# Kernel optimization log

Hardware: AMD Instinct MI355X
Metric: run time of the kernel (lower is better)

## Reference

```python
import jax, jax.numpy as jnp
import numpy as np

D_MODEL = 1024
H = 16
D_K = D_MODEL // H


def setup_inputs() -> dict:
    key = jax.random.key(0)
    ks = jax.random.split(key, 8)
    B, S = 4, 2048
    q = jax.random.normal(ks[0], (B, S, D_MODEL), dtype=jnp.float32)
    k = jax.random.normal(ks[1], (B, S, D_MODEL), dtype=jnp.float32)
    v = jax.random.normal(ks[2], (B, S, D_MODEL), dtype=jnp.float32)
    scale = 1.0 / np.sqrt(D_MODEL)
    W_q = jax.random.normal(ks[3], (H, D_MODEL, D_K), dtype=jnp.float32) * scale
    W_k = jax.random.normal(ks[4], (H, D_MODEL, D_K), dtype=jnp.float32) * scale
    W_v = jax.random.normal(ks[5], (H, D_MODEL, D_K), dtype=jnp.float32) * scale
    W_o = jax.random.normal(ks[6], (D_MODEL, H * D_K), dtype=jnp.float32) * scale
    b_o = jax.random.normal(ks[7], (D_MODEL,), dtype=jnp.float32) * 0.01
    return {"q": q, "k": k, "v": v, "W_q": W_q, "W_k": W_k, "W_v": W_v, "W_o": W_o, "b_o": b_o}


def reference(q, k, v, W_q, W_k, W_v, W_o, b_o):
    # Per-head projections: [B,S,D] x [H,D,dk] -> [H,B,S,dk]
    qh = jnp.einsum('bsd,hdk->hbsk', q, W_q)
    kh = jnp.einsum('bsd,hdk->hbsk', k, W_k)
    vh = jnp.einsum('bsd,hdk->hbsk', v, W_v)
    # Scaled dot-product attention (full score matrix, as in original)
    scores = jnp.einsum('hbsk,hbtk->hbst', qh, kh) / jnp.sqrt(jnp.asarray(D_K, qh.dtype))
    attn = jax.nn.softmax(scores, axis=-1)
    out = jnp.einsum('hbst,hbtk->hbsk', attn, vh)  # [H,B,S,dk]
    # torch.cat(chunks along head dim, dim=2): head-major feature concat -> [B,S,H*dk]
    out = jnp.transpose(out, (1, 2, 0, 3)).reshape(q.shape[0], q.shape[1], H * D_K)
    return out @ W_o.T + b_o
```

## Files before the change

kernel.cpp:

```cpp
#include <hip/hip_runtime.h>

#define S_LEN 2048

typedef __attribute__((ext_vector_type(8))) short v8s;
typedef __attribute__((ext_vector_type(4))) short v4s;
typedef __attribute__((ext_vector_type(4))) float f32x4;
typedef __attribute__((ext_vector_type(4))) unsigned short v4us;
typedef __attribute__((ext_vector_type(4))) unsigned int v4u;

static __device__ __forceinline__ unsigned short f2bf(float x){
  unsigned u = __builtin_bit_cast(unsigned, x);
  u = (u + 0x7fffu + ((u >> 16) & 1u)) >> 16;
  return (unsigned short)u;
}

static __device__ __forceinline__ unsigned pk2(float a, float b){
  unsigned ua = __builtin_bit_cast(unsigned, a) + 0x8000u;
  unsigned ub = __builtin_bit_cast(unsigned, b) + 0x8000u;
  return __builtin_amdgcn_perm(ub, ua, 0x07060302u);
}

static __device__ __forceinline__ void gload16(const void* g, void* l){
  __builtin_amdgcn_global_load_lds((const __attribute__((address_space(1))) void*)g,
                                   (__attribute__((address_space(3))) void*)l, 16, 0, 0);
}

static __device__ __forceinline__ unsigned lds_off(const void* p){
  return (unsigned)(unsigned long long)(__attribute__((address_space(3))) const void*)p;
}

__global__ void conv_w(const float* __restrict__ Wq, const float* __restrict__ Wk,
                       const float* __restrict__ Wv, const float* __restrict__ Wo,
                       unsigned short* __restrict__ outW){
  int i = blockIdx.x*256 + threadIdx.x;
  const int stride = gridDim.x*256;
  for(; i < 4*1048576; i += stride){
    if (i < 3*1048576){
      int which = i >> 20;
      int rem = i & 1048575;
      const float* W = which==0 ? Wq : (which==1 ? Wk : Wv);
      float v = W[rem];
      if (which == 0) v *= 0.18033688011112042f;
      int h = rem >> 16, d = (rem >> 6) & 1023, kk = rem & 63;
      outW[(which<<20) + (((h<<6)+kk)<<10) + d] = f2bf(v);
    } else {
      outW[i] = f2bf(Wo[i - 3*1048576]);
    }
  }
}

__global__ __launch_bounds__(256,2) void gemm_proj(
    const float* __restrict__ Aq, const float* __restrict__ Ak, const float* __restrict__ Avv,
    const unsigned short* __restrict__ Wtb,
    unsigned short* __restrict__ C0, unsigned short* __restrict__ C1, unsigned short* __restrict__ C2){
  __shared__ unsigned short Als[128*64];
  __shared__ unsigned short Bls[128*64];
  const int tid = threadIdx.x;
  const int l = tid & 63, w = tid >> 6;
  const int z = blockIdx.z;
  const float* Af = (z==0) ? Aq : ((z==1) ? Ak : Avv);
  unsigned short* Cb = (z==0) ? C0 : ((z==1) ? C1 : C2);
  int lid = blockIdx.y*8 + blockIdx.x;
  int nid = (lid & 7)*64 + (lid >> 3);
  const int tx = nid & 7, ty = nid >> 3;
  const int m0 = ty*128, n0 = tx*128;
  const int wr = w >> 1, wc = w & 1;

  f32x4 zero = {0.f,0.f,0.f,0.f};
  f32x4 acc[4][4];
  #pragma unroll
  for(int i=0;i<4;i++){
    #pragma unroll
    for(int j=0;j<4;j++) acc[i][j] = zero;
  }

  const int xorm = (l&7)<<4;
  const int g8 = (l>>4)<<3;
  const int rsub = l>>3, csub = l&7;
  const float* Abase = Af + m0*1024;
  const unsigned short* Bbase = Wtb + z*1048576 + n0*1024;

  float4 ar[8];
  #pragma unroll
  for(int i=0;i<4;i++){
    int c = w*4+i, r = c*8+rsub;
    const float4* src = (const float4*)(Abase + r*1024 + csub*8);
    ar[2*i] = src[0]; ar[2*i+1] = src[1];
  }

  for(int kt=0; kt<16; ++kt){
    const int k0 = kt*64;
    __builtin_amdgcn_sched_barrier(0);
    #pragma unroll
    for(int i=0;i<4;i++){
      int c = w*4+i, r = c*8+rsub, col = csub ^ (r&7);
      gload16(Bbase + r*1024 + k0 + col*8, (void*)&Bls[c*512]);
    }
    __builtin_amdgcn_sched_barrier(0);
    #pragma unroll
    for(int i=0;i<4;i++){
      int c = w*4+i, r = c*8+rsub;
      v4u o = { pk2(ar[2*i].x, ar[2*i].y), pk2(ar[2*i].z, ar[2*i].w),
                pk2(ar[2*i+1].x, ar[2*i+1].y), pk2(ar[2*i+1].z, ar[2*i+1].w) };
      *(v4u*)&Als[c*512 + rsub*64 + ((csub ^ (r&7))<<3)] = o;
    }
    __builtin_amdgcn_sched_barrier(0);
    if (kt < 15){
      #pragma unroll
      for(int i=0;i<4;i++){
        int c = w*4+i, r = c*8+rsub;
        const float4* src = (const float4*)(Abase + r*1024 + (k0+64) + csub*8);
        ar[2*i] = src[0]; ar[2*i+1] = src[1];
      }
      __builtin_amdgcn_sched_barrier(0);
      asm volatile("s_waitcnt vmcnt(8) lgkmcnt(0)" ::: "memory");
    } else {
      asm volatile("s_waitcnt vmcnt(0) lgkmcnt(0)" ::: "memory");
    }
    __builtin_amdgcn_s_barrier();
    __builtin_amdgcn_sched_barrier(0);

    const char* Ab = (const char*)Als;
    const char* Bb = (const char*)Bls;
    #pragma unroll
    for(int kk=0; kk<2; ++kk){
      v8s af[4], bfr[4];
      #pragma unroll
      for(int mf=0; mf<4; ++mf){
        int rb = (wr*64 + mf*16 + (l&15))*128;
        v4s lo = *(const v4s*)(Ab + rb + ((kk*64 + g8) ^ xorm));
        v4s hi = *(const v4s*)(Ab + rb + ((kk*64 + 32 + g8) ^ xorm));
        af[mf] = __builtin_shufflevector(lo, hi, 0,1,2,3,4,5,6,7);
      }
      #pragma unroll
      for(int nf=0; nf<4; ++nf){
        int rb = (wc*64 + nf*16 + (l&15))*128;
        v4s lo = *(const v4s*)(Bb + rb + ((kk*64 + g8) ^ xorm));
        v4s hi = *(const v4s*)(Bb + rb + ((kk*64 + 32 + g8) ^ xorm));
        bfr[nf] = __builtin_shufflevector(lo, hi, 0,1,2,3,4,5,6,7);
      }
      #pragma unroll
      for(int mf=0; mf<4; ++mf){
        #pragma unroll
        for(int nf=0; nf<4; ++nf)
          acc[mf][nf] = __builtin_amdgcn_mfma_f32_16x16x32_bf16(af[mf], bfr[nf], acc[mf][nf], 0,0,0);
      }
    }
    __builtin_amdgcn_sched_barrier(0);
    __builtin_amdgcn_s_barrier();
  }

  const int g4 = (l>>4)<<2;
  #pragma unroll
  for(int mf=0; mf<4; ++mf){
    int rowb = m0 + wr*64 + mf*16 + g4;
    #pragma unroll
    for(int nf=0; nf<4; ++nf){
      int col = n0 + wc*64 + nf*16 + (l&15);
      #pragma unroll
      for(int r=0;r<4;++r)
        Cb[(rowb+r)*1024 + col] = f2bf(acc[mf][nf][r]);
    }
  }
}

template<int EPI>
__global__ __launch_bounds__(256,2) void gemm_bt(const unsigned short* __restrict__ A,
                                                 const unsigned short* __restrict__ Bt,
                                                 void* __restrict__ Cout,
                                                 const float* __restrict__ bias){
  __shared__ unsigned short Als[128*64];
  __shared__ unsigned short Bls[128*64];
  const int tid = threadIdx.x;
  const int l = tid & 63, w = tid >> 6;
  int lid = blockIdx.y*8 + blockIdx.x;
  int nid = (lid & 7)*64 + (lid >> 3);
  const int tx = nid & 7, ty = nid >> 3;
  const int m0 = ty*128, n0 = tx*128;
  const int wr = w >> 1, wc = w & 1;

  f32x4 zero = {0.f,0.f,0.f,0.f};
  f32x4 acc[4][4];
  #pragma unroll
  for(int i=0;i<4;i++){
    #pragma unroll
    for(int j=0;j<4;j++) acc[i][j] = zero;
  }

  const int xorm = (l&7)<<4;
  const int g8 = (l>>4)<<3;
  const int rsub = l>>3, csub = l&7;
  const unsigned short* Abase = A + m0*1024;
  const unsigned short* Bbase = Bt + n0*1024;

  for(int kt=0; kt<16; ++kt){
    const int k0 = kt*64;
    #pragma unroll
    for(int i=0;i<4;i++){
      int c = w*4+i, r = c*8+rsub, col = csub ^ (r&7);
      gload16(Abase + r*1024 + k0 + col*8, (void*)&Als[c*512]);
    }
    #pragma unroll
    for(int i=0;i<4;i++){
      int c = w*4+i, r = c*8+rsub, col = csub ^ (r&7);
      gload16(Bbase + r*1024 + k0 + col*8, (void*)&Bls[c*512]);
    }
    __syncthreads();
    const char* Ab = (const char*)Als;
    const char* Bb = (const char*)Bls;
    #pragma unroll
    for(int kk=0; kk<2; ++kk){
      v8s af[4], bfr[4];
      #pragma unroll
      for(int mf=0; mf<4; ++mf){
        int rb = (wr*64 + mf*16 + (l&15))*128;
        v4s lo = *(const v4s*)(Ab + rb + ((kk*64 + g8) ^ xorm));
        v4s hi = *(const v4s*)(Ab + rb + ((kk*64 + 32 + g8) ^ xorm));
        af[mf] = __builtin_shufflevector(lo, hi, 0,1,2,3,4,5,6,7);
      }
      #pragma unroll
      for(int nf=0; nf<4; ++nf){
        int rb = (wc*64 + nf*16 + (l&15))*128;
        v4s lo = *(const v4s*)(Bb + rb + ((kk*64 + g8) ^ xorm));
        v4s hi = *(const v4s*)(Bb + rb + ((kk*64 + 32 + g8) ^ xorm));
        bfr[nf] = __builtin_shufflevector(lo, hi, 0,1,2,3,4,5,6,7);
      }
      #pragma unroll
      for(int mf=0; mf<4; ++mf){
        #pragma unroll
        for(int nf=0; nf<4; ++nf)
          acc[mf][nf] = __builtin_amdgcn_mfma_f32_16x16x32_bf16(af[mf], bfr[nf], acc[mf][nf], 0,0,0);
      }
    }
    __syncthreads();
  }

  const int g4 = (l>>4)<<2;
  if (EPI == 0){
    unsigned short* C = (unsigned short*)Cout;
    #pragma unroll
    for(int mf=0; mf<4; ++mf){
      int rowb = m0 + wr*64 + mf*16 + g4;
      #pragma unroll
      for(int nf=0; nf<4; ++nf){
        int col = n0 + wc*64 + nf*16 + (l&15);
        #pragma unroll
        for(int r=0;r<4;++r)
          C[(rowb+r)*1024 + col] = f2bf(acc[mf][nf][r]);
      }
    }
  } else {
    float* C = (float*)Cout;
    #pragma unroll
    for(int mf=0; mf<4; ++mf){
      int rowb = m0 + wr*64 + mf*16 + g4;
      #pragma unroll
      for(int nf=0; nf<4; ++nf){
        int col = n0 + wc*64 + nf*16 + (l&15);
        float bv = bias[col];
        #pragma unroll
        for(int r=0;r<4;++r)
          C[(rowb+r)*1024 + col] = acc[mf][nf][r] + bv;
      }
    }
  }
}

__global__ __launch_bounds__(256,2) void attn_fwd(const unsigned short* __restrict__ Q,
                                                  const unsigned short* __restrict__ K,
                                                  const unsigned short* __restrict__ V,
                                                  unsigned short* __restrict__ O){
  __shared__ unsigned short KVls[2][2][64*64];
  const int tid = threadIdx.x;
  const int l = tid & 63, w = tid >> 6;
  int lid = blockIdx.y*16 + blockIdx.x;
  int nid = (lid & 7)*128 + (lid >> 3);
  const int qb = nid & 15, bh = nid >> 4;
  const int b = bh >> 4, h = bh & 15;
  const int base = b*S_LEN*1024 + h*64;
  const int q0 = qb*128;
  const int xorm = (l&7)<<4, g8 = (l>>4)<<3, g4 = (l>>4)<<2;
  const int rsub = l>>3, csub = l&7;

  auto stage_kv = [&](int kt2, int buf){
    const int k0 = kt2*64;
    #pragma unroll
    for(int i=0;i<2;i++){
      int c = w*2+i, r = c*8+rsub, col = csub ^ (r&7);
      gload16(K + base + (k0+r)*1024 + col*8, (void*)&KVls[buf][0][c*512]);
    }
    #pragma unroll
    for(int i=0;i<2;i++){
      int c = w*2+i;
      int e0 = c*512 + l*8;
      int kg = e0>>10, dg = (e0>>8)&3, kin = (e0>>4)&15, din = e0&15;
      gload16(V + base + (k0 + kg*16 + kin)*1024 + dg*16 + din, (void*)&KVls[buf][1][c*512]);
    }
  };

  #pragma unroll
  for(int i=0;i<4;i++){
    int c = w*4+i, r = c*8+rsub, col = csub ^ (r&7);
    gload16(Q + base + (q0+r)*1024 + col*8, (void*)&KVls[1][0][c*512]);
  }
  stage_kv(0, 0);
  __syncthreads();

  v8s qf[2][2];
  {
    const char* Qb = (const char*)&KVls[1][0][0];
    #pragma unroll
    for(int qh=0; qh<2; ++qh){
      int rb = (w*32 + qh*16 + (l&15))*128;
      #pragma unroll
      for(int t=0;t<2;t++){
        v4s lo = *(const v4s*)(Qb + rb + ((t*64 + g8) ^ xorm));
        v4s hi = *(const v4s*)(Qb + rb + ((t*64 + 32 + g8) ^ xorm));
        qf[qh][t] = __builtin_shufflevector(lo, hi, 0,1,2,3,4,5,6,7);
      }
    }
  }
  __builtin_amdgcn_sched_barrier(0);
  __syncthreads();

  f32x4 zero = {0.f,0.f,0.f,0.f};
  f32x4 oacc[2][4];
  #pragma unroll
  for(int qh=0;qh<2;qh++){
    #pragma unroll
    for(int nf=0;nf<4;nf++) oacc[qh][nf] = zero;
  }
  float lsum[2] = {0.f, 0.f};
  const unsigned vbase0 = lds_off(&KVls[0][1][0]) + l*8;
  const unsigned vbase1 = lds_off(&KVls[1][1][0]) + l*8;

  int cur = 0;
  for(int kt=0; kt<32; ++kt){
    if (kt < 31) stage_kv(kt+1, cur^1);

    const char* Kb = (const char*)&KVls[cur][0][0];
    f32x4 sf[2][4];
    #pragma unroll
    for(int mf=0;mf<4;mf++){
      int rb = (mf*16 + (l&15))*128;
      v8s kf[2];
      #pragma unroll
      for(int t=0;t<2;t++){
        v4s lo = *(const v4s*)(Kb + rb + ((t*64 + g8) ^ xorm));
        v4s hi = *(const v4s*)(Kb + rb + ((t*64 + 32 + g8) ^ xorm));
        kf[t] = __builtin_shufflevector(lo, hi, 0,1,2,3,4,5,6,7);
      }
      #pragma unroll
      for(int qh=0;qh<2;qh++){
        sf[qh][mf] = __builtin_amdgcn_mfma_f32_16x16x32_bf16(kf[0], qf[qh][0], zero, 0,0,0);
        sf[qh][mf] = __builtin_amdgcn_mfma_f32_16x16x32_bf16(kf[1], qf[qh][1], sf[qh][mf], 0,0,0);
      }
    }

    const unsigned vb_sel = cur ? vbase1 : vbase0;
    v4s vtr[2][2][4];
    #define TRR(T,H,N,OFF) asm volatile("ds_read_b64_tr_b16 %0, %1 offset:" #OFF \
                     : "=v"(vtr[T][H][N]) : "v"(vb_sel) : "memory")
    TRR(0,0,0,0);    TRR(0,0,1,512);  TRR(0,0,2,1024); TRR(0,0,3,1536);
    TRR(0,1,0,2048); TRR(0,1,1,2560); TRR(0,1,2,3072); TRR(0,1,3,3584);
    TRR(1,0,0,4096); TRR(1,0,1,4608); TRR(1,0,2,5120); TRR(1,0,3,5632);
    TRR(1,1,0,6144); TRR(1,1,1,6656); TRR(1,1,2,7168); TRR(1,1,3,7680);
    #undef TRR

    v8s pa[2][2];
    #pragma unroll
    for(int qh=0;qh<2;qh++){
      unsigned pd[2][4];
      float ls = 0.f;
      #pragma unroll
      for(int mf=0;mf<4;mf++){
        float e0 = __builtin_amdgcn_exp2f(sf[qh][mf][0]);
        float e1 = __builtin_amdgcn_exp2f(sf[qh][mf][1]);
        float e2 = __builtin_amdgcn_exp2f(sf[qh][mf][2]);
        float e3 = __builtin_amdgcn_exp2f(sf[qh][mf][3]);
        ls += (e0+e1)+(e2+e3);
        int t = mf>>1, hf = mf&1;
        pd[t][hf*2+0] = pk2(e0, e1);
        pd[t][hf*2+1] = pk2(e2, e3);
      }
      lsum[qh] += ls;
      #pragma unroll
      for(int t=0;t<2;t++){
        v4u u = { pd[t][0], pd[t][1], pd[t][2], pd[t][3] };
        pa[qh][t] = __builtin_bit_cast(v8s, u);
      }
    }

    asm volatile("s_waitcnt lgkmcnt(0)" ::: "memory");
    __builtin_amdgcn_sched_barrier(0);
    __builtin_amdgcn_s_setprio(1);
    #pragma unroll
    for(int t=0;t<2;t++){
      #pragma unroll
      for(int nf=0;nf<4;nf++){
        v8s vb = __builtin_shufflevector(vtr[t][0][nf], vtr[t][1][nf], 0,1,2,3,4,5,6,7);
        #pragma unroll
        for(int qh=0;qh<2;qh++)
          oacc[qh][nf] = __builtin_amdgcn_mfma_f32_16x16x32_bf16(pa[qh][t], vb, oacc[qh][nf], 0,0,0);
      }
    }
    __builtin_amdgcn_s_setprio(0);
    __syncthreads();
    cur ^= 1;
  }

  #pragma unroll
  for(int qh=0;qh<2;qh++){
    float s = lsum[qh];
    s += __shfl_xor(s, 16, 64);
    s += __shfl_xor(s, 32, 64);
    float i0 = 1.f/__shfl(s, g4+0, 64);
    float i1 = 1.f/__shfl(s, g4+1, 64);
    float i2 = 1.f/__shfl(s, g4+2, 64);
    float i3 = 1.f/__shfl(s, g4+3, 64);
    const int row = q0 + w*32 + qh*16 + g4;
    #pragma unroll
    for(int nf=0;nf<4;nf++){
      int col = nf*16 + (l&15);
      O[base + (row+0)*1024 + col] = f2bf(oacc[qh][nf][0]*i0);
      O[base + (row+1)*1024 + col] = f2bf(oacc[qh][nf][1]*i1);
      O[base + (row+2)*1024 + col] = f2bf(oacc[qh][nf][2]*i2);
      O[base + (row+3)*1024 + col] = f2bf(oacc[qh][nf][3]*i3);
    }
  }
}

extern "C" void kernel_launch(void* const* d_in, const int* in_sizes, int n_in,
                              void* d_out, int out_size, void* d_ws, size_t ws_size,
                              hipStream_t stream) {
  (void)in_sizes; (void)n_in; (void)out_size;
  const float* q  = (const float*)d_in[0];
  const float* k  = (const float*)d_in[1];
  const float* v  = (const float*)d_in[2];
  const float* Wq = (const float*)d_in[3];
  const float* Wk = (const float*)d_in[4];
  const float* Wv = (const float*)d_in[5];
  const float* Wo = (const float*)d_in[6];
  const float* bo = (const float*)d_in[7];

  if (ws_size < (size_t)37748736*2) return;
  unsigned short* ws  = (unsigned short*)d_ws;
  unsigned short* Qh  = ws;
  unsigned short* Kh  = ws +  8388608;
  unsigned short* Vh  = ws + 16777216;
  unsigned short* AO  = ws + 25165824;
  unsigned short* Wt  = ws + 33554432;
  unsigned short* Wob = Wt + 3145728;

  conv_w<<<dim3(2048), dim3(256), 0, stream>>>(Wq, Wk, Wv, Wo, Wt);

  gemm_proj<<<dim3(8,64,3), dim3(256), 0, stream>>>(q, k, v, Wt, Qh, Kh, Vh);

  attn_fwd<<<dim3(16,64), dim3(256), 0, stream>>>(Qh, Kh, Vh, AO);

  gemm_bt<1><<<dim3(8,64), dim3(256), 0, stream>>>(AO, Wob, d_out, bo);
}
```

Measured before the change: 233.1 us.

## Double-buffer LDS tiles in projection GEMM to overlap loads with MFMA

Result: no change. 231.0 us (-0.9%).

```diff
diff --git a/kernel.cpp b/kernel.cpp
--- a/kernel.cpp
+++ b/kernel.cpp
@@ -53,8 +53,8 @@
     const float* __restrict__ Aq, const float* __restrict__ Ak, const float* __restrict__ Avv,
     const unsigned short* __restrict__ Wtb,
     unsigned short* __restrict__ C0, unsigned short* __restrict__ C1, unsigned short* __restrict__ C2){
-  __shared__ unsigned short Als[128*64];
-  __shared__ unsigned short Bls[128*64];
+  __shared__ unsigned short Als[2][128*64];
+  __shared__ unsigned short Bls[2][128*64];
   const int tid = threadIdx.x;
   const int l = tid & 63, w = tid >> 6;
   const int z = blockIdx.z;
@@ -83,45 +83,61 @@
   float4 ar[8];
   #pragma unroll
   for(int i=0;i<4;i++){
+    int c = w*4+i, r = c*8+rsub, col = csub ^ (r&7);
+    gload16(Bbase + r*1024 + col*8, (void*)&Bls[0][c*512]);
+  }
+  #pragma unroll
+  for(int i=0;i<4;i++){
     int c = w*4+i, r = c*8+rsub;
     const float4* src = (const float4*)(Abase + r*1024 + csub*8);
     ar[2*i] = src[0]; ar[2*i+1] = src[1];
   }
-
+  #pragma unroll
+  for(int i=0;i<4;i++){
+    int c = w*4+i, r = c*8+rsub;
+    v4u o = { pk2(ar[2*i].x, ar[2*i].y), pk2(ar[2*i].z, ar[2*i].w),
+              pk2(ar[2*i+1].x, ar[2*i+1].y), pk2(ar[2*i+1].z, ar[2*i+1].w) };
+    *(v4u*)&Als[0][c*512 + rsub*64 + ((csub ^ (r&7))<<3)] = o;
+  }
+  #pragma unroll
+  for(int i=0;i<4;i++){
+    int c = w*4+i, r = c*8+rsub;
+    const float4* src = (const float4*)(Abase + r*1024 + 64 + csub*8);
+    ar[2*i] = src[0]; ar[2*i+1] = src[1];
+  }
+  asm volatile("s_waitcnt lgkmcnt(0)" ::: "memory");
+  __builtin_amdgcn_s_barrier();
+
+  int cur = 0;
   for(int kt=0; kt<16; ++kt){
-    const int k0 = kt*64;
-    __builtin_amdgcn_sched_barrier(0);
-    #pragma unroll
-    for(int i=0;i<4;i++){
-      int c = w*4+i, r = c*8+rsub, col = csub ^ (r&7);
-      gload16(Bbase + r*1024 + k0 + col*8, (void*)&Bls[c*512]);
-    }
-    __builtin_amdgcn_sched_barrier(0);
-    #pragma unroll
-    for(int i=0;i<4;i++){
-      int c = w*4+i, r = c*8+rsub;
-      v4u o = { pk2(ar[2*i].x, ar[2*i].y), pk2(ar[2*i].z, ar[2*i].w),
-                pk2(ar[2*i+1].x, ar[2*i+1].y), pk2(ar[2*i+1].z, ar[2*i+1].w) };
-      *(v4u*)&Als[c*512 + rsub*64 + ((csub ^ (r&7))<<3)] = o;
-    }
     __builtin_amdgcn_sched_barrier(0);
     if (kt < 15){
       #pragma unroll
       for(int i=0;i<4;i++){
         int c = w*4+i, r = c*8+rsub;
-        const float4* src = (const float4*)(Abase + r*1024 + (k0+64) + csub*8);
-        ar[2*i] = src[0]; ar[2*i+1] = src[1];
+        v4u o = { pk2(ar[2*i].x, ar[2*i].y), pk2(ar[2*i].z, ar[2*i].w),
+                  pk2(ar[2*i+1].x, ar[2*i+1].y), pk2(ar[2*i+1].z, ar[2*i+1].w) };
+        *(v4u*)&Als[cur^1][c*512 + rsub*64 + ((csub ^ (r&7))<<3)] = o;
       }
       __builtin_amdgcn_sched_barrier(0);
-      asm volatile("s_waitcnt vmcnt(8) lgkmcnt(0)" ::: "memory");
-    } else {
-      asm volatile("s_waitcnt vmcnt(0) lgkmcnt(0)" ::: "memory");
-    }
-    __builtin_amdgcn_s_barrier();
-    __builtin_amdgcn_sched_barrier(0);
-
-    const char* Ab = (const char*)Als;
-    const char* Bb = (const char*)Bls;
+      #pragma unroll
+      for(int i=0;i<4;i++){
+        int c = w*4+i, r = c*8+rsub, col = csub ^ (r&7);
+        gload16(Bbase + r*1024 + (kt+1)*64 + col*8, (void*)&Bls[cur^1][c*512]);
+      }
+      __builtin_amdgcn_sched_barrier(0);
+      if (kt < 14){
+        #pragma unroll
+        for(int i=0;i<4;i++){
+          int c = w*4+i, r = c*8+rsub;
+          const float4* src = (const float4*)(Abase + r*1024 + (kt+2)*64 + csub*8);
+          ar[2*i] = src[0]; ar[2*i+1] = src[1];
+        }
+        __builtin_amdgcn_sched_barrier(0);
+      }
+    }
+    const char* Ab = (const char*)&Als[cur][0];
+    const char* Bb = (const char*)&Bls[cur][0];
     #pragma unroll
     for(int kk=0; kk<2; ++kk){
       v8s af[4], bfr[4];
@@ -147,7 +163,15 @@
       }
     }
     __builtin_amdgcn_sched_barrier(0);
-    __builtin_amdgcn_s_barrier();
+    if (kt < 15){
+      if (kt < 14){
+        asm volatile("s_waitcnt vmcnt(8) lgkmcnt(0)" ::: "memory");
+      } else {
+        asm volatile("s_waitcnt vmcnt(0) lgkmcnt(0)" ::: "memory");
+      }
+      __builtin_amdgcn_s_barrier();
+    }
+    cur ^= 1;
   }
 
   const int g4 = (l>>4)<<2;
```
